# Kernel optimization log

Measured on AMD Instinct MI355X. Metric: run time of the kernel, lower is better.

Reference implementation:

```python
import jax, jax.numpy as jnp
import numpy as np
import math

B, N = 1, 768
C_S, C_Z, C_H, H, P_QK, P_V = 256, 128, 128, 8, 8, 12
EPS, INF, LN_EPS = 1e-8, 1e5, 1e-5


def _quat_to_rot(q):
    # q: [..., 4] normalized quaternion (w, x, y, z) -> [..., 3, 3]
    w, x, y, z = jnp.moveaxis(q, -1, 0)
    r = jnp.stack([
        1 - 2 * (y * y + z * z), 2 * (x * y - w * z), 2 * (x * z + w * y),
        2 * (x * y + w * z), 1 - 2 * (x * x + z * z), 2 * (y * z - w * x),
        2 * (x * z - w * y), 2 * (y * z + w * x), 1 - 2 * (x * x + y * y),
    ], axis=-1)
    return r.reshape(q.shape[:-1] + (3, 3))


def _ln(x, g, b):
    mu = x.mean(-1, keepdims=True)
    var = ((x - mu) ** 2).mean(-1, keepdims=True)
    return (x - mu) * jax.lax.rsqrt(var + LN_EPS) * g + b


def setup_inputs():
    key = jax.random.key(0)
    ks = jax.random.split(key, 20)
    inp = {}
    inp['s'] = jax.random.normal(ks[0], (B, N, C_S), jnp.float32)
    inp['p'] = jax.random.normal(ks[1], (B, N, N, C_Z), jnp.float32)
    q = jax.random.normal(ks[2], (B, N, 4), jnp.float32)
    inp['rot'] = _quat_to_rot(q / jnp.linalg.norm(q, axis=-1, keepdims=True))
    inp['trans'] = 10.0 * jax.random.normal(ks[3], (B, N, 3), jnp.float32)
    inp['mask'] = jnp.ones((B, N), jnp.float32)
    concat_dim = H * C_H + H * P_V * 4 + H * C_Z
    dims = {'q': (H * C_H, C_S), 'kv': (2 * H * C_H, C_S), 'qp': (H * P_QK * 3, C_S),
            'kvp': (H * (P_QK + P_V) * 3, C_S), 'pb': (H, C_Z), 'o': (C_S, concat_dim),
            't1': (C_S, C_S), 't2': (C_S, C_S), 't3': (C_S, C_S), 'bb': (6, C_S)}
    i = 4
    for nm, (do, di) in dims.items():
        k1, k2 = jax.random.split(ks[i]); i += 1
        inp['W' + nm] = 0.02 * jax.random.normal(k1, (do, di), jnp.float32)
        inp['b' + nm] = 0.02 * jax.random.normal(k2, (do,), jnp.float32)
    inp['head_w'] = 0.1 * jax.random.normal(ks[i], (H,), jnp.float32)
    inp['g1'] = jnp.ones((C_S,), jnp.float32)
    inp['be1'] = jnp.zeros((C_S,), jnp.float32)
    inp['g2'] = jnp.ones((C_S,), jnp.float32)
    inp['be2'] = jnp.zeros((C_S,), jnp.float32)
    return inp


def reference(s, p, rot, trans, mask, Wq, bq, Wkv, bkv, Wqp, bqp, Wkvp, bkvp,
              Wpb, bpb, Wo, bo, Wt1, bt1, Wt2, bt2, Wt3, bt3, Wbb, bbb,
              head_w, g1, be1, g2, be2):
    # ---------------- Invariant Point Attention ----------------
    q = (s @ Wq.T + bq).reshape(B, N, H, C_H)
    kv = (s @ Wkv.T + bkv).reshape(B, N, H, 2 * C_H)
    k, v = kv[..., :C_H], kv[..., C_H:]
    # points: linear output is coordinate-major (x-block, y-block, z-block)
    qp = (s @ Wqp.T + bqp).reshape(B, N, 3, H, P_QK)
    qp = jnp.einsum('bnij,bnjhp->bnhpi', rot, qp) + trans[:, :, None, None, :]
    kvp = (s @ Wkvp.T + bkvp).reshape(B, N, 3, H, P_QK + P_V)
    kvp = jnp.einsum('bnij,bnjhp->bnhpi', rot, kvp) + trans[:, :, None, None, :]
    kp, vp = kvp[..., :P_QK, :], kvp[..., P_QK:, :]
    bias_p = p @ Wpb.T + bpb  # [B,N,N,H]
    a = jnp.einsum('bihc,bjhc->bhij', q, k) * math.sqrt(1.0 / (3 * C_H))
    a = a + math.sqrt(1.0 / 3) * jnp.transpose(bias_p, (0, 3, 1, 2))
    d2 = ((qp[:, :, None] - kp[:, None]) ** 2).sum(-1)  # [B,N,N,H,Pqk]
    hw = jax.nn.softplus(head_w) * math.sqrt(1.0 / (3 * (P_QK * 9.0 / 2)))
    pt_att = -0.5 * (d2 * hw[None, None, None, :, None]).sum(-1)  # [B,N,N,H]
    m2 = mask[:, :, None] * mask[:, None, :]
    a = a + jnp.transpose(pt_att, (0, 3, 1, 2)) + (INF * (m2 - 1.0))[:, None]
    att = jax.nn.softmax(a, axis=-1)  # [B,H,N,N]
    o = jnp.einsum('bhij,bjhc->bihc', att, v).reshape(B, N, H * C_H)
    opt = jnp.einsum('bhij,bjhpx->bihpx', att, vp)  # [B,N,H,Pv,3] global
    opt = jnp.einsum('bnji,bnhpj->bnhpi', rot, opt - trans[:, :, None, None, :])
    opt_norm = jnp.sqrt((opt ** 2).sum(-1) + EPS).reshape(B, N, H * P_V)
    opt_flat = jnp.moveaxis(opt.reshape(B, N, H * P_V, 3), -1, -2).reshape(B, N, 3 * H * P_V)
    opair = jnp.einsum('bhij,bijz->bihz', att, p).reshape(B, N, H * C_Z)
    ipa_out = jnp.concatenate([o, opt_flat, opt_norm, opair], -1) @ Wo.T + bo
    # residual + dropout(eval: identity) + LayerNorm
    s1 = _ln(s + ipa_out, g1, be1)
    # ---------------- StructureTransition (1 layer) ----------------
    x = jax.nn.relu(s1 @ Wt1.T + bt1)
    x = jax.nn.relu(x @ Wt2.T + bt2)
    s2 = _ln(s1 + (x @ Wt3.T + bt3), g2, be2)
    # ---------------- BackboneUpdate + masked quaternion compose ----------------
    upd = (s2 @ Wbb.T + bbb) * mask[..., None]  # [B,N,6]
    qvec = jnp.concatenate([jnp.ones(upd.shape[:-1] + (1,), upd.dtype), upd[..., :3]], -1)
    qvec = qvec / jnp.linalg.norm(qvec, axis=-1, keepdims=True)
    rot_new = jnp.einsum('bnij,bnjk->bnik', rot, _quat_to_rot(qvec))
    trans_new = trans + jnp.einsum('bnij,bnj->bni', rot, upd[..., 3:])
    return (s2, rot_new, trans_new)
```

## Files before the change

### kernel.cpp

```cpp
#include <hip/hip_runtime.h>
#include <hip/hip_bf16.h>
#include <math.h>

#define NN 768
#define CS 256
#define CZ 128
#define CH 128
#define HH 8
#define PQK 8
#define PV 12
#define CONCAT 2432
#define ATT_HSTRIDE (768*768)

typedef __bf16 v8bf __attribute__((ext_vector_type(8)));
typedef __bf16 v4bf __attribute__((ext_vector_type(4)));
typedef float  v4f  __attribute__((ext_vector_type(4)));

__device__ inline unsigned short f2bf(float f) {
    union { float f; unsigned u; } v; v.f = f;
    unsigned r = v.u + 0x7FFFu + ((v.u >> 16) & 1u);
    return (unsigned short)(r >> 16);
}
__device__ inline float bf2f(unsigned short u) {
    union { unsigned u; float f; } v; v.u = ((unsigned)u) << 16; return v.f;
}

#define NCVT 9
struct CvtDesc {
    const float* src[NCVT];
    unsigned short* dst[NCVT];
    int nelem[NCVT];
    int blk_start[NCVT + 1];
};

__global__ __launch_bounds__(256) void cvt_many(CvtDesc d)
{
    int b = blockIdx.x;
    int seg = 0;
    #pragma unroll
    for (int i = 0; i < NCVT - 1; i++) if (b >= d.blk_start[i + 1]) seg = i + 1;
    int local = b - d.blk_start[seg];
    int base = local * 2048 + threadIdx.x;
    const float* s = d.src[seg];
    unsigned short* o = d.dst[seg];
    int n = d.nelem[seg];
    #pragma unroll
    for (int r = 0; r < 8; r++) {
        int idx = base + r * 256;
        if (idx < n) o[idx] = f2bf(s[idx]);
    }
}

struct ProjDesc {
    const unsigned short* W[4];
    const float* bias[4];
    unsigned short* dstb[4];
    float* dstf[4];
// ... 100 lines not shown
        v8bf b0 = *(const v8bf*)&Ws[wc + fr][fc];
        v8bf b1 = *(const v8bf*)&Ws[wc + 16 + fr][fc];
        acc[0][0] = __builtin_amdgcn_mfma_f32_16x16x32_bf16(a0, b0, acc[0][0], 0, 0, 0);
        acc[0][1] = __builtin_amdgcn_mfma_f32_16x16x32_bf16(a0, b1, acc[0][1], 0, 0, 0);
        acc[1][0] = __builtin_amdgcn_mfma_f32_16x16x32_bf16(a1, b0, acc[1][0], 0, 0, 0);
        acc[1][1] = __builtin_amdgcn_mfma_f32_16x16x32_bf16(a1, b1, acc[1][1], 0, 0, 0);
        __syncthreads();
    }
    int mrow = (lane >> 4) * 4;
    #pragma unroll
    for (int mi = 0; mi < 2; mi++) {
        #pragma unroll
        for (int ni = 0; ni < 2; ni++) {
            int d = bd + wc + ni * 16 + fr;
            if (d < D) {
                #pragma unroll
                for (int r = 0; r < 4; r++) {
                    int m = bi + wr + mi * 16 + mrow + r;
                    float v = acc[mi][ni][r];
                    if (SPLITK > 1) {
                        atomicAdd(&C[(size_t)m * ldc + d], v);
                    } else {
                        v += bias[d];
                        if (RELU) v = fmaxf(v, 0.f);
                        if (MODE != 2) C[(size_t)m * ldc + d] = v;
                        if (MODE >= 1) Cb[(size_t)m * ldc + d] = f2bf(v);
                    }
                }
            }
        }
    }
}

__global__ __launch_bounds__(256) void ipa_init_kernel(
    const float* __restrict__ bo, float* __restrict__ ipa)
{
    ipa[blockIdx.x * 256 + threadIdx.x] = bo[threadIdx.x];
}

__global__ void rotate_kernel(
    const float* __restrict__ qpraw, const float* __restrict__ kvpraw,
    const float* __restrict__ rot, const float* __restrict__ trans,
    unsigned short* __restrict__ qph, unsigned short* __restrict__ qpl,
    unsigned short* __restrict__ kph, unsigned short* __restrict__ kpl,
    unsigned short* __restrict__ Vc)
{
    int id = blockIdx.x*256 + threadIdx.x;
    if (id >= NN*HH*28) return;
    int i = id / (HH*28);
    int rem = id % (HH*28);
    int h = rem / 28;
    int idx = rem % 28;
    const float* R = rot + i*9;
    const float* T = trans + i*3;
    float s0, s1, s2;
    if (idx < 8) {
        s0 = qpraw[i*192 +   0 + h*8 + idx];
        s1 = qpraw[i*192 +  64 + h*8 + idx];
        s2 = qpraw[i*192 + 128 + h*8 + idx];
    } else {
        int pp = idx - 8;
        s0 = kvpraw[i*480 +   0 + h*20 + pp];
        s1 = kvpraw[i*480 + 160 + h*20 + pp];
        s2 = kvpraw[i*480 + 320 + h*20 + pp];
    }
    float ov[3];
    ov[0] = R[0]*s0 + R[1]*s1 + R[2]*s2 + T[0];
    ov[1] = R[3]*s0 + R[4]*s1 + R[5]*s2 + T[1];
    ov[2] = R[6]*s0 + R[7]*s1 + R[8]*s2 + T[2];
    if (idx < 8) {
        #pragma unroll
        for (int x = 0; x < 3; x++) {
            unsigned short hi = f2bf(ov[x]);
            qph[i*256 + h*32 + idx*3 + x] = hi;
            qpl[i*256 + h*32 + idx*3 + x] = f2bf(ov[x] - bf2f(hi));
        }
        if (idx == 0) {
            #pragma unroll
            for (int m = 24; m < 32; m++) { qph[i*256+h*32+m] = 0; qpl[i*256+h*32+m] = 0; }
        }
    } else if (idx < 16) {
        int pp = idx - 8;
        #pragma unroll
        for (int x = 0; x < 3; x++) {
            unsigned short hi = f2bf(ov[x]);
            kph[i*256 + h*32 + pp*3 + x] = hi;
            kpl[i*256 + h*32 + pp*3 + x] = f2bf(ov[x] - bf2f(hi));
        }
        if (idx == 8) {
            #pragma unroll
            for (int m = 24; m < 32; m++) { kph[i*256+h*32+m] = 0; kpl[i*256+h*32+m] = 0; }
        }
    } else {
        int ppv = idx - 16;
        #pragma unroll
        for (int x = 0; x < 3; x++)
            Vc[((size_t)h*192 + 128 + ppv*3 + x)*768 + i] = f2bf(ov[x]);
    }
}

__global__ __launch_bounds__(256) void vtrans_kernel(
    const unsigned short* __restrict__ kv_bf, unsigned short* __restrict__ Vc)
{
    __shared__ unsigned short tile[32][136];
    int h = blockIdx.x & 7, jt = blockIdx.x >> 3;
    int t = threadIdx.x;
    int r = t >> 3, c0 = (t & 7) * 16;
    const unsigned short* src = kv_bf + (size_t)(jt*32 + r)*2048 + h*256 + 128 + c0;
    *(int4*)&tile[r][c0]     = *(const int4*)src;
    *(int4*)&tile[r][c0 + 8] = *(const int4*)(src + 8);
    __syncthreads();
    int c = t >> 1, jh = (t & 1) * 16;
    unsigned short tmp[16];
    #pragma unroll
    for (int k = 0; k < 16; k++) tmp[k] = tile[jh + k][c];
    unsigned short* dst = Vc + ((size_t)h*192 + c)*768 + jt*32 + jh;
    *(int4*)dst       = *(int4*)&tmp[0];
    *(int4*)(dst + 8) = *(int4*)&tmp[8];
}

__global__ __launch_bounds__(256) void logits_mfma(
    const unsigned short* __restrict__ q_bf, const unsigned short* __restrict__ kv_bf,
    const unsigned short* __restrict__ qph, const unsigned short* __restrict__ qpl,
    const unsigned short* __restrict__ kph, const unsigned short* __restrict__ kpl,
    const float* __restrict__ mask, const float* __restrict__ head_w,
    float* __restrict__ att)
{
    __shared__ unsigned short Qs[64][136];
    __shared__ unsigned short Ks[64][136];
    __shared__ unsigned short Aph[64][40], Apl[64][40], Bph[64][40], Bpl[64][40];
    __shared__ float Qss[64], Kss[64], Mi[64], Mj[64];
    int h = blockIdx.z;
    int i0 = blockIdx.y * 64, j0 = blockIdx.x * 64;
    int tid = threadIdx.x, lane = tid & 63, wid = tid >> 6;
    int wr = (wid >> 1) * 32, wc = (wid & 1) * 32;
    int r = tid >> 2, cq = (tid & 3) * 32;
    const unsigned short* qg = q_bf  + (size_t)(i0 + r)*1024 + h*128 + cq;
    const unsigned short* kg = kv_bf + (size_t)(j0 + r)*2048 + h*256 + cq;
    #pragma unroll
    for (int kk = 0; kk < 4; kk++) {
        *(int4*)&Qs[r][cq + kk*8] = *(const int4*)(qg + kk*8);
        *(int4*)&Ks[r][cq + kk*8] = *(const int4*)(kg + kk*8);
    }
    int cp = (tid & 3) * 8;
    *(int4*)&Aph[r][cp] = *(const int4*)(qph + (size_t)(i0 + r)*256 + h*32 + cp);
    *(int4*)&Apl[r][cp] = *(const int4*)(qpl + (size_t)(i0 + r)*256 + h*32 + cp);
    *(int4*)&Bph[r][cp] = *(const int4*)(kph + (size_t)(j0 + r)*256 + h*32 + cp);
    *(int4*)&Bpl[r][cp] = *(const int4*)(kpl + (size_t)(j0 + r)*256 + h*32 + cp);
    if (tid < 64) {
        Mi[tid] = mask[i0 + tid];
        Mj[tid] = mask[j0 + tid];
    }
    __syncthreads();
    if (tid < 64) {
        float qs2 = 0.f, ks2 = 0.f;
        #pragma unroll
        for (int m = 0; m < 24; m++) {
            float qv = bf2f(Aph[tid][m]) + bf2f(Apl[tid][m]);
            float kv = bf2f(Bph[tid][m]) + bf2f(Bpl[tid][m]);
// ... 12 lines not shown
        aqk[0][0] = __builtin_amdgcn_mfma_f32_16x16x32_bf16(a0, b0, aqk[0][0], 0, 0, 0);
        aqk[0][1] = __builtin_amdgcn_mfma_f32_16x16x32_bf16(a0, b1, aqk[0][1], 0, 0, 0);
        aqk[1][0] = __builtin_amdgcn_mfma_f32_16x16x32_bf16(a1, b0, aqk[1][0], 0, 0, 0);
        aqk[1][1] = __builtin_amdgcn_mfma_f32_16x16x32_bf16(a1, b1, aqk[1][1], 0, 0, 0);
    }
    {
        v8bf ah0 = *(const v8bf*)&Aph[wr + fr][fc];
        v8bf ah1 = *(const v8bf*)&Aph[wr + 16 + fr][fc];
        v8bf al0 = *(const v8bf*)&Apl[wr + fr][fc];
        v8bf al1 = *(const v8bf*)&Apl[wr + 16 + fr][fc];
        v8bf bh0 = *(const v8bf*)&Bph[wc + fr][fc];
        v8bf bh1 = *(const v8bf*)&Bph[wc + 16 + fr][fc];
        v8bf bl0 = *(const v8bf*)&Bpl[wc + fr][fc];
        v8bf bl1 = *(const v8bf*)&Bpl[wc + 16 + fr][fc];
        ap[0][0] = __builtin_amdgcn_mfma_f32_16x16x32_bf16(ah0, bh0, ap[0][0], 0, 0, 0);
        ap[0][1] = __builtin_amdgcn_mfma_f32_16x16x32_bf16(ah0, bh1, ap[0][1], 0, 0, 0);
        ap[1][0] = __builtin_amdgcn_mfma_f32_16x16x32_bf16(ah1, bh0, ap[1][0], 0, 0, 0);
        ap[1][1] = __builtin_amdgcn_mfma_f32_16x16x32_bf16(ah1, bh1, ap[1][1], 0, 0, 0);
        ap[0][0] = __builtin_amdgcn_mfma_f32_16x16x32_bf16(ah0, bl0, ap[0][0], 0, 0, 0);
        ap[0][1] = __builtin_amdgcn_mfma_f32_16x16x32_bf16(ah0, bl1, ap[0][1], 0, 0, 0);
        ap[1][0] = __builtin_amdgcn_mfma_f32_16x16x32_bf16(ah1, bl0, ap[1][0], 0, 0, 0);
        ap[1][1] = __builtin_amdgcn_mfma_f32_16x16x32_bf16(ah1, bl1, ap[1][1], 0, 0, 0);
        ap[0][0] = __builtin_amdgcn_mfma_f32_16x16x32_bf16(al0, bh0, ap[0][0], 0, 0, 0);
        ap[0][1] = __builtin_amdgcn_mfma_f32_16x16x32_bf16(al0, bh1, ap[0][1], 0, 0, 0);
        ap[1][0] = __builtin_amdgcn_mfma_f32_16x16x32_bf16(al1, bh0, ap[1][0], 0, 0, 0);
        ap[1][1] = __builtin_amdgcn_mfma_f32_16x16x32_bf16(al1, bh1, ap[1][1], 0, 0, 0);
    }
    __syncthreads();
    float hx = head_w[h];
    float sp = (hx > 20.f) ? hx : log1pf(__expf(hx));
    float hw = sp * 0.09622504486493764f;
    const float scale_qk = 0.05103103630798288f;
    int mrow = (lane >> 4) * 4;
    #pragma unroll
    for (int mi = 0; mi < 2; mi++) {
        #pragma unroll
        for (int ni = 0; ni < 2; ni++) {
            int jl = wc + ni*16 + fr;
            #pragma unroll
            for (int rr = 0; rr < 4; rr++) {
                int il = wr + mi*16 + mrow + rr;
                size_t aidx = (size_t)h*ATT_HSTRIDE + (size_t)(i0 + il)*768 + (j0 + jl);
                att[aidx] = aqk[mi][ni][rr]*scale_qk + hw*ap[mi][ni][rr]
                          - 0.5f*hw*(Qss[il] + Kss[jl])
                          + 100000.0f*(Mi[il]*Mj[jl] - 1.0f);
            }
        }
    }
}

__global__ __launch_bounds__(256) void fused_p3_kernel(
    const float* __restrict__ att0,
    const float* __restrict__ p,
    const float* __restrict__ Wpb, const float* __restrict__ bpb,
    unsigned short* __restrict__ att_bf,
    float* __restrict__ linv,
    unsigned short* __restrict__ concat)
{
    __shared__ unsigned short ptile[64][132];
    __shared__ unsigned short wt[16][72];
    __shared__ float bpb_s[8], m8[8], inv_s[8], lsum_w[4][8];

    int i = blockIdx.x;
    int tid = threadIdx.x, lane = tid & 63, wid = tid >> 6;
    int fr = lane & 15, fc = (lane >> 4) * 8;
    int mrow = (lane >> 4) * 4;

    for (int idx = tid; idx < 16*72; idx += 256) ((unsigned short*)wt)[idx] = 0;
    if (tid < 8) bpb_s[tid] = bpb[tid];

    v8bf aW[4];
    #pragma unroll
    for (int ks = 0; ks < 4; ks++) {
        v8bf v = {};
        if (fr < 8) {
            const float* wp = Wpb + fr*128 + ks*32 + fc;
            float4 w0 = *(const float4*)wp;
            float4 w1 = *(const float4*)(wp + 4);
            v[0] = (__bf16)w0.x; v[1] = (__bf16)w0.y; v[2] = (__bf16)w0.z; v[3] = (__bf16)w0.w;
            v[4] = (__bf16)w1.x; v[5] = (__bf16)w1.y; v[6] = (__bf16)w1.z; v[7] = (__bf16)w1.w;
        }
        aW[ks] = v;
    }

    {
        const float* abase = att0 + (size_t)i*768;
        #pragma unroll
        for (int hh = 0; hh < 2; hh++) {
            int h = wid*2 + hh;
            const float* row = abase + (size_t)h*ATT_HSTRIDE;
            float m = -3.0e38f;
            #pragma unroll
            for (int e = 0; e < 12; e++) m = fmaxf(m, row[lane + e*64]);
            #pragma unroll
            for (int d2 = 1; d2 < 64; d2 <<= 1) m = fmaxf(m, __shfl_xor(m, d2));
            if (lane == 0) m8[h] = m;
        }
    }
    __syncthreads();
    float m0a[4], m0b[4];
    #pragma unroll
    for (int r = 0; r < 4; r++) { m0a[r] = m8[r]; m0b[r] = m8[4 + r]; }
    float m0l[4];
    #pragma unroll
    for (int r = 0; r < 4; r++) m0l[r] = (mrow == 0) ? m0a[r] : m0b[r];

    const float* pbase = p + (size_t)i*98304;
    float4 pfA[4], pfB[4];
    #pragma unroll
    for (int r = 0; r < 4; r++) {
        int idx = r*256 + tid;
        const float* src = pbase + (idx >> 4)*128 + (idx & 15)*8;
        pfA[r] = *(const float4*)src;
        pfB[r] = *(const float4*)(src + 4);
    }

    v4f accD[2] = {};
    float lacc[4] = {0.f, 0.f, 0.f, 0.f};
    const float sqrt13 = 0.57735026918962576f;
    bool expo = (mrow < 8);

    for (int t64 = 0; t64 < 12; t64++) {
        int j0 = t64 * 64;
        #pragma unroll
        for (int r = 0; r < 4; r++) {
            int idx = r*256 + tid;
            int j = idx >> 4, zo = (idx & 15) * 8;
            v4bf lo, hi;
            lo[0] = (__bf16)pfA[r].x; lo[1] = (__bf16)pfA[r].y;
            lo[2] = (__bf16)pfA[r].z; lo[3] = (__bf16)pfA[r].w;
            hi[0] = (__bf16)pfB[r].x; hi[1] = (__bf16)pfB[r].y;
            hi[2] = (__bf16)pfB[r].z; hi[3] = (__bf16)pfB[r].w;
            *(v4bf*)&ptile[j][zo]     = lo;
            *(v4bf*)&ptile[j][zo + 4] = hi;
        }
        if (t64 < 11) {
            int j0n = j0 + 64;
            #pragma unroll
            for (int r = 0; r < 4; r++) {
                int idx = r*256 + tid;
                const float* src = pbase + (size_t)(j0n + (idx >> 4))*128 + (idx & 15)*8;
                pfA[r] = *(const float4*)src;
                pfB[r] = *(const float4*)(src + 4);
            }
        }
        __syncthreads();

        float a0v[4];
        if (expo) {
            int j = 16*wid + fr;
            #pragma unroll
            for (int r = 0; r < 4; r++)
                a0v[r] = att0[((size_t)(mrow + r)*768 + i)*768 + j0 + j];
        }

        v4f bd = {};
        #pragma unroll
        for (int ks = 0; ks < 4; ks++) {
            int c = ks*32 + fc;
            v4bf blo = *(const v4bf*)&ptile[16*wid + fr][c];
            v4bf bhi = *(const v4bf*)&ptile[16*wid + fr][c + 4];
            v8bf b;
            b[0]=blo[0]; b[1]=blo[1]; b[2]=blo[2]; b[3]=blo[3];
            b[4]=bhi[0]; b[5]=bhi[1]; b[6]=bhi[2]; b[7]=bhi[3];
            bd = __builtin_amdgcn_mfma_f32_16x16x32_bf16(aW[ks], b, bd, 0, 0, 0);
        }

        if (expo) {
            int j = 16*wid + fr;
            float w8[4];
            #pragma unroll
            for (int r = 0; r < 4; r++) {
                int h = mrow + r;
                float L = a0v[r] + sqrt13*(bd[r] + bpb_s[h]);
// ... 8 lines not shown
            }
            #pragma unroll
            for (int m = 1; m < 16; m <<= 1) {
                #pragma unroll
                for (int r = 0; r < 4; r++) w8[r] += __shfl_xor(w8[r], m);
            }
            #pragma unroll
            for (int r = 0; r < 4; r++) lacc[r] += w8[r];
        }
        __syncthreads();

        #pragma unroll
        for (int mm = 0; mm < 2; mm++) {
            int zcol = (2*wid + mm)*16 + fr;
            #pragma unroll
            for (int ks = 0; ks < 2; ks++) {
                v8bf b;
                #pragma unroll
                for (int kk = 0; kk < 8; kk++)
                    b[kk] = *(const __bf16*)&ptile[ks*32 + fc + kk][zcol];
                v8bf a = *(const v8bf*)&wt[fr][ks*32 + fc];
                accD[mm] = __builtin_amdgcn_mfma_f32_16x16x32_bf16(a, b, accD[mm], 0, 0, 0);
            }
        }
        __syncthreads();
    }

    if (fr == 0 && expo) {
        #pragma unroll
        for (int r = 0; r < 4; r++) lsum_w[wid][mrow + r] = lacc[r];
    }
    __syncthreads();
    if (tid < 8) {
        float l = lsum_w[0][tid] + lsum_w[1][tid] + lsum_w[2][tid] + lsum_w[3][tid];
        float iv = 1.0f / l;
        inv_s[tid] = iv;
        linv[(size_t)tid*768 + i] = iv;
    }
    __syncthreads();
    if (expo) {
        #pragma unroll
        for (int mm = 0; mm < 2; mm++) {
            int z = (2*wid + mm)*16 + fr;
            #pragma unroll
            for (int r = 0; r < 4; r++) {
                int h = mrow + r;
                concat[(size_t)i*CONCAT + 1408 + h*128 + z] = f2bf(accD[mm][r] * inv_s[h]);
            }
        }
    }
}

__global__ __launch_bounds__(256) void attvc_mfma(
    const unsigned short* __restrict__ att_bf, const unsigned short* __restrict__ Vc,
    const float* __restrict__ linv, const float* __restrict__ rot,
    const float* __restrict__ trans, unsigned short* __restrict__ concat)
{
    __shared__ unsigned short As[64][72];
    __shared__ unsigned short Bs[64][72];
    int h = blockIdx.z;
    int i0 = blockIdx.y * 64, nd0 = blockIdx.x * 64;
    int tid = threadIdx.x, lane = tid & 63, wid = tid >> 6;
    int wr = (wid >> 1) * 32, wc = (wid & 1) * 32;
    int r = tid >> 2, c8 = (tid & 3) * 16;
    int fr = lane & 15, fc = (lane >> 4) * 8;
    v4f acc[2][2] = {};
    for (int k0 = 0; k0 < 768; k0 += 64) {
        const unsigned short* ag = att_bf + ((size_t)h*768 + i0 + r)*768 + k0 + c8;
        const unsigned short* bg = Vc + ((size_t)h*192 + nd0 + r)*768 + k0 + c8;
        *(int4*)&As[r][c8]     = *(const int4*)ag;
        *(int4*)&As[r][c8 + 8] = *(const int4*)(ag + 8);
        *(int4*)&Bs[r][c8]     = *(const int4*)bg;
        *(int4*)&Bs[r][c8 + 8] = *(const int4*)(bg + 8);
        __syncthreads();
        #pragma unroll
        for (int ks = 0; ks < 2; ks++) {
            v8bf a0 = *(const v8bf*)&As[wr + fr][ks*32 + fc];
            v8bf a1 = *(const v8bf*)&As[wr + 16 + fr][ks*32 + fc];
            v8bf b0 = *(const v8bf*)&Bs[wc + fr][ks*32 + fc];
            v8bf b1 = *(const v8bf*)&Bs[wc + 16 + fr][ks*32 + fc];
            acc[0][0] = __builtin_amdgcn_mfma_f32_16x16x32_bf16(a0, b0, acc[0][0], 0, 0, 0);
            acc[0][1] = __builtin_amdgcn_mfma_f32_16x16x32_bf16(a0, b1, acc[0][1], 0, 0, 0);
// ... 32 lines not shown
                int c = wc + ni*16 + fr;
                if (c < 36) {
                    #pragma unroll
                    for (int rr = 0; rr < 4; rr++) {
                        int rl = wr + mi*16 + mrow + rr;
                        opt_s[rl*36 + c] = acc[mi][ni][rr] * lv[mi][rr];
                    }
                }
            }
        }
        __syncthreads();
        for (int it = tid; it < 768; it += 256) {
            int rl = it / 12, pp = it % 12;
            int i = i0 + rl;
            const float* R = rot + i*9;
            const float* T = trans + i*3;
            float y0 = opt_s[rl*36 + pp*3 + 0] - T[0];
            float y1 = opt_s[rl*36 + pp*3 + 1] - T[1];
            float y2 = opt_s[rl*36 + pp*3 + 2] - T[2];
            float o0 = R[0]*y0 + R[3]*y1 + R[6]*y2;
            float o1 = R[1]*y0 + R[4]*y1 + R[7]*y2;
            float o2 = R[2]*y0 + R[5]*y1 + R[8]*y2;
            float nrm = sqrtf(o0*o0 + o1*o1 + o2*o2 + 1e-8f);
            int hp = h*12 + pp;
            unsigned short* cb = concat + (size_t)i*CONCAT;
            cb[1024 +   0 + hp] = f2bf(o0);
            cb[1024 +  96 + hp] = f2bf(o1);
            cb[1024 + 192 + hp] = f2bf(o2);
            cb[1312 + hp] = f2bf(nrm);
        }
    }
}

template<int BF>
__global__ __launch_bounds__(256) void add_ln_kernel(
    const float* __restrict__ A, const float* __restrict__ Bv,
    const float* __restrict__ g, const float* __restrict__ be,
    float* __restrict__ out, unsigned short* __restrict__ outb)
{
    int i = blockIdx.x, t = threadIdx.x;
    float x = A[i*256 + t] + Bv[i*256 + t];
    __shared__ float red[4];
    float v = x;
    #pragma unroll
    for (int m = 1; m < 64; m <<= 1) v += __shfl_xor(v, m);
    if ((t & 63) == 0) red[t >> 6] = v;
    __syncthreads();
    float mu = (red[0] + red[1] + red[2] + red[3]) * (1.0f/256.0f);
    __syncthreads();
    float d = x - mu;
    float v2 = d*d;
    #pragma unroll
    for (int m = 1; m < 64; m <<= 1) v2 += __shfl_xor(v2, m);
    if ((t & 63) == 0) red[t >> 6] = v2;
    __syncthreads();
    float var = (red[0] + red[1] + red[2] + red[3]) * (1.0f/256.0f);
    float o = d * (1.0f/sqrtf(var + 1e-5f)) * g[t] + be[t];
    out[i*256 + t] = o;
    if (BF) outb[i*256 + t] = f2bf(o);
}

__global__ __launch_bounds__(256) void upd_frame_kernel(
    const float* __restrict__ s2, const float* __restrict__ Wbb,
    const float* __restrict__ bbb, const float* __restrict__ mask,
    const float* __restrict__ rot, const float* __restrict__ trans,
    float* __restrict__ rot_out, float* __restrict__ trans_out)
{
    int i = blockIdx.x, t = threadIdx.x;
    __shared__ float row[256];
    __shared__ float upd_s[6];
    row[t] = s2[i*256 + t];
    __syncthreads();
    if (t < 6) {
        float acc = bbb[t];
        #pragma unroll 8
        for (int c = 0; c < 256; c++) acc += row[c]*Wbb[t*256 + c];
        upd_s[t] = acc * mask[i];
    }
    __syncthreads();
    if (t == 0) {
        float u0 = upd_s[0], u1 = upd_s[1], u2 = upd_s[2];
        float t0 = upd_s[3], t1 = upd_s[4], t2 = upd_s[5];
        float n = sqrtf(1.f + u0*u0 + u1*u1 + u2*u2);
        float w = 1.f/n, x = u0/n, y = u1/n, z = u2/n;
        float R[3][3];
        R[0][0] = 1.f - 2.f*(y*y + z*z); R[0][1] = 2.f*(x*y - w*z);       R[0][2] = 2.f*(x*z + w*y);
        R[1][0] = 2.f*(x*y + w*z);       R[1][1] = 1.f - 2.f*(x*x + z*z); R[1][2] = 2.f*(y*z - w*x);
        R[2][0] = 2.f*(x*z - w*y);       R[2][1] = 2.f*(y*z + w*x);       R[2][2] = 1.f - 2.f*(x*x + y*y);
        const float* Ri = rot + i*9;
        #pragma unroll
        for (int a = 0; a < 3; a++) {
            #pragma unroll
            for (int b = 0; b < 3; b++) {
                float acc = 0.f;
                #pragma unroll
                for (int j = 0; j < 3; j++) acc += Ri[a*3+j]*R[j][b];
                rot_out[i*9 + a*3 + b] = acc;
            }
            trans_out[i*3 + a] = trans[i*3 + a] + Ri[a*3+0]*t0 + Ri[a*3+1]*t1 + Ri[a*3+2]*t2;
        }
    }
}

extern "C" void kernel_launch(void* const* d_in, const int* in_sizes, int n_in,
                              void* d_out, int out_size, void* d_ws, size_t ws_size,
                              hipStream_t stream)
{
    const float* s      = (const float*)d_in[0];
    const float* p      = (const float*)d_in[1];
    const float* rot    = (const float*)d_in[2];
    const float* trans  = (const float*)d_in[3];
    const float* mask   = (const float*)d_in[4];
    const float* Wq     = (const float*)d_in[5];
    const float* bq     = (const float*)d_in[6];
    const float* Wkv    = (const float*)d_in[7];
// ... 3 lines not shown
    const float* Wkvp   = (const float*)d_in[11];
    const float* bkvp   = (const float*)d_in[12];
    const float* Wpb    = (const float*)d_in[13];
    const float* bpb    = (const float*)d_in[14];
    const float* Wo     = (const float*)d_in[15];
    const float* bo     = (const float*)d_in[16];
    const float* Wt1    = (const float*)d_in[17];
    const float* bt1    = (const float*)d_in[18];
    const float* Wt2    = (const float*)d_in[19];
    const float* bt2    = (const float*)d_in[20];
    const float* Wt3    = (const float*)d_in[21];
    const float* bt3    = (const float*)d_in[22];
    const float* Wbb    = (const float*)d_in[23];
    const float* bbb    = (const float*)d_in[24];
    const float* head_w = (const float*)d_in[25];
    const float* g1     = (const float*)d_in[26];
    const float* be1    = (const float*)d_in[27];
    const float* g2     = (const float*)d_in[28];
    const float* be2    = (const float*)d_in[29];

    float* out = (float*)d_out;
    char*  wsb = (char*)d_ws;

    size_t off = 0;
    auto alloc = [&](size_t bytes) -> char* {
        char* ptr = wsb + off;
        off += (bytes + 255) & ~(size_t)255;
        return ptr;
    };
    float* qpraw   = (float*)alloc((size_t)NN*192*4);
    float* kvpraw  = (float*)alloc((size_t)NN*480*4);
    float* att     = (float*)alloc((size_t)8*768*768*4);
    float* ipa     = (float*)alloc((size_t)NN*256*4);
    float* s1      = (float*)alloc((size_t)NN*256*4);
    float* y3      = (float*)alloc((size_t)NN*256*4);
    float* linv    = (float*)alloc((size_t)8*768*4);
    unsigned short* s_bf    = (unsigned short*)alloc((size_t)NN*256*2);
    unsigned short* Wq_bf   = (unsigned short*)alloc((size_t)1024*256*2);
    unsigned short* Wkv_bf  = (unsigned short*)alloc((size_t)2048*256*2);
    unsigned short* Wqp_bf  = (unsigned short*)alloc((size_t)192*256*2);
    unsigned short* Wkvp_bf = (unsigned short*)alloc((size_t)480*256*2);
    unsigned short* Wo_bf   = (unsigned short*)alloc((size_t)256*2432*2);
    unsigned short* Wt1_bf  = (unsigned short*)alloc((size_t)256*256*2);
    unsigned short* Wt2_bf  = (unsigned short*)alloc((size_t)256*256*2);
    unsigned short* Wt3_bf  = (unsigned short*)alloc((size_t)256*256*2);
    unsigned short* q_bf    = (unsigned short*)alloc((size_t)NN*1024*2);
    unsigned short* kv_bf   = (unsigned short*)alloc((size_t)NN*2048*2);
    unsigned short* qph     = (unsigned short*)alloc((size_t)NN*256*2);
    unsigned short* qpl     = (unsigned short*)alloc((size_t)NN*256*2);
    unsigned short* kph     = (unsigned short*)alloc((size_t)NN*256*2);
    unsigned short* kpl     = (unsigned short*)alloc((size_t)NN*256*2);
    unsigned short* Vc      = (unsigned short*)alloc((size_t)8*192*768*2);
    unsigned short* att_bf  = (unsigned short*)alloc((size_t)8*768*768*2);
    unsigned short* concat  = (unsigned short*)alloc((size_t)NN*CONCAT*2);
    unsigned short* s1b     = (unsigned short*)alloc((size_t)NN*256*2);
    unsigned short* x1b     = (unsigned short*)alloc((size_t)NN*256*2);
    unsigned short* x2b     = (unsigned short*)alloc((size_t)NN*256*2);

    ipa_init_kernel<<<768, 256, 0, stream>>>(bo, ipa);

    CvtDesc cd;
    const float* csrc[NCVT]    = {s, Wq, Wkv, Wqp, Wkvp, Wo, Wt1, Wt2, Wt3};
    unsigned short* cdst[NCVT] = {s_bf, Wq_bf, Wkv_bf, Wqp_bf, Wkvp_bf, Wo_bf, Wt1_bf, Wt2_bf, Wt3_bf};
    int csz[NCVT] = {NN*256, 1024*256, 2048*256, 192*256, 480*256, 256*2432, 256*256, 256*256, 256*256};
    int cum = 0;
    for (int i2 = 0; i2 < NCVT; i2++) {
        cd.src[i2] = csrc[i2]; cd.dst[i2] = cdst[i2]; cd.nelem[i2] = csz[i2];
        cd.blk_start[i2] = cum;
        cum += (csz[i2] + 2047) / 2048;
    }
    cd.blk_start[NCVT] = cum;
    cvt_many<<<cum, 256, 0, stream>>>(cd);

    ProjDesc pd;
    pd.W[0] = Wq_bf;   pd.bias[0] = bq;   pd.dstb[0] = q_bf;   pd.dstf[0] = nullptr; pd.D[0] = 1024; pd.ldc[0] = 1024; pd.mode[0] = 2;
    pd.W[1] = Wkv_bf;  pd.bias[1] = bkv;  pd.dstb[1] = kv_bf;  pd.dstf[1] = nullptr; pd.D[1] = 2048; pd.ldc[1] = 2048; pd.mode[1] = 2;
    pd.W[2] = Wqp_bf;  pd.bias[2] = bqp;  pd.dstb[2] = nullptr; pd.dstf[2] = qpraw;  pd.D[2] = 192;  pd.ldc[2] = 192;  pd.mode[2] = 0;
    pd.W[3] = Wkvp_bf; pd.bias[3] = bkvp; pd.dstb[3] = nullptr; pd.dstf[3] = kvpraw; pd.D[3] = 480;  pd.ldc[3] = 480;  pd.mode[3] = 0;
    pd.blk_start[0] = 0; pd.blk_start[1] = 16; pd.blk_start[2] = 48; pd.blk_start[3] = 51; pd.blk_start[4] = 59;
    proj_all<<<dim3(59, 12), 256, 0, stream>>>(s_bf, pd);

    rotate_kernel<<<(NN*HH*28 + 255)/256, 256, 0, stream>>>(
        qpraw, kvpraw, rot, trans, qph, qpl, kph, kpl, Vc);
    vtrans_kernel<<<8*24, 256, 0, stream>>>(kv_bf, Vc);

    logits_mfma<<<dim3(12, 12, 8), 256, 0, stream>>>(
        q_bf, kv_bf, qph, qpl, kph, kpl, mask, head_w, att);
    fused_p3_kernel<<<768, 256, 0, stream>>>(att, p, Wpb, bpb, att_bf, linv, concat);

    attvc_mfma<<<dim3(3, 12, 8), 256, 0, stream>>>(att_bf, Vc, linv, rot, trans, concat);

    mfma_gemm<4,0,0><<<dim3(4,12,4), 256, 0, stream>>>(concat, Wo_bf, nullptr, ipa, nullptr, 256, 2432, 256);
    add_ln_kernel<1><<<768, 256, 0, stream>>>(s, ipa, g1, be1, s1, s1b);

    mfma_gemm<1,2,1><<<dim3(4,12), 256, 0, stream>>>(s1b, Wt1_bf, bt1, nullptr, x1b, 256, 256, 256);
    mfma_gemm<1,2,1><<<dim3(4,12), 256, 0, stream>>>(x1b, Wt2_bf, bt2, nullptr, x2b, 256, 256, 256);
    mfma_gemm<1,0,0><<<dim3(4,12), 256, 0, stream>>>(x2b, Wt3_bf, bt3, y3, nullptr, 256, 256, 256);
    add_ln_kernel<0><<<768, 256, 0, stream>>>(s1, y3, g2, be2, out, nullptr);

    upd_frame_kernel<<<768, 256, 0, stream>>>(out, Wbb, bbb, mask, rot, trans,
                                              out + (size_t)NN*256, out + (size_t)NN*256 + (size_t)NN*9);
}
```

Before: 195.1 us.

## Fuse prep and tail kernels, move row-max into logits, split pair pass

Merges the rotate and V-transpose kernels into one launch. The softmax row max is now computed inside the logits kernel through atomicMax on order-preserving encoded floats, so the pair kernel no longer rereads att for the max. The pair-bias/opair kernel is split over two j-halves for more parallelism, and a new reduce kernel combines the partial sums and outputs. The LN, transition MLP, LN and frame-update stages are fused into one 24-block tail kernel, and bias init is replaced by a memset with bo added in the tail. The changes cut launches and att traffic, but the tail runs on only 24 blocks and the split adds partial-sum buffers.

```diff
diff --git a/kernel.cpp b/kernel.cpp
--- a/kernel.cpp
+++ b/kernel.cpp
@@ -23,6 +23,14 @@
 }
 __device__ inline float bf2f(unsigned short u) {
     union { unsigned u; float f; } v; v.u = ((unsigned)u) << 16; return v.f;
+}
+__device__ inline unsigned encf(float f) {
+    unsigned u = __float_as_uint(f);
+    return (u >> 31) ? ~u : (u | 0x80000000u);
+}
+__device__ inline float decf(unsigned e) {
+    unsigned u = (e >> 31) ? (e & 0x7FFFFFFFu) : ~e;
+    return __uint_as_float(u);
 }
 
 #define NCVT 9
@@ -189,91 +197,85 @@
     }
 }
 
-__global__ __launch_bounds__(256) void ipa_init_kernel(
-    const float* __restrict__ bo, float* __restrict__ ipa)
-{
-    ipa[blockIdx.x * 256 + threadIdx.x] = bo[threadIdx.x];
-}
-
-__global__ void rotate_kernel(
+__global__ __launch_bounds__(256) void prep2_kernel(
     const float* __restrict__ qpraw, const float* __restrict__ kvpraw,
     const float* __restrict__ rot, const float* __restrict__ trans,
+    const unsigned short* __restrict__ kv_bf,
     unsigned short* __restrict__ qph, unsigned short* __restrict__ qpl,
     unsigned short* __restrict__ kph, unsigned short* __restrict__ kpl,
     unsigned short* __restrict__ Vc)
 {
-    int id = blockIdx.x*256 + threadIdx.x;
-    if (id >= NN*HH*28) return;
-    int i = id / (HH*28);
-    int rem = id % (HH*28);
-    int h = rem / 28;
-    int idx = rem % 28;
-    const float* R = rot + i*9;
-    const float* T = trans + i*3;
-    float s0, s1, s2;
-    if (idx < 8) {
-        s0 = qpraw[i*192 +   0 + h*8 + idx];
-        s1 = qpraw[i*192 +  64 + h*8 + idx];
-        s2 = qpraw[i*192 + 128 + h*8 + idx];
+    __shared__ unsigned short tile[32][136];
+    int bx = blockIdx.x;
+    int t = threadIdx.x;
+    if (bx < 672) {
+        int id = bx*256 + t;
+        int i = id / (HH*28);
+        int rem = id % (HH*28);
+        int h = rem / 28;
+        int idx = rem % 28;
+        const float* R = rot + i*9;
+        const float* T = trans + i*3;
+        float s0, s1, s2;
+        if (idx < 8) {
+            s0 = qpraw[i*192 +   0 + h*8 + idx];
+            s1 = qpraw[i*192 +  64 + h*8 + idx];
+            s2 = qpraw[i*192 + 128 + h*8 + idx];
+        } else {
+            int pp = idx - 8;
+            s0 = kvpraw[i*480 +   0 + h*20 + pp];
+            s1 = kvpraw[i*480 + 160 + h*20 + pp];
+            s2 = kvpraw[i*480 + 320 + h*20 + pp];
+        }
+        float ov[3];
+        ov[0] = R[0]*s0 + R[1]*s1 + R[2]*s2 + T[0];
+        ov[1] = R[3]*s0 + R[4]*s1 + R[5]*s2 + T[1];
+        ov[2] = R[6]*s0 + R[7]*s1 + R[8]*s2 + T[2];
+        if (idx < 8) {
+            #pragma unroll
+            for (int x = 0; x < 3; x++) {
+                unsigned short hi = f2bf(ov[x]);
+                qph[i*256 + h*32 + idx*3 + x] = hi;
+                qpl[i*256 + h*32 + idx*3 + x] = f2bf(ov[x] - bf2f(hi));
+            }
+            if (idx == 0) {
+                #pragma unroll
+                for (int m = 24; m < 32; m++) { qph[i*256+h*32+m] = 0; qpl[i*256+h*32+m] = 0; }
+            }
+        } else if (idx < 16) {
+            int pp = idx - 8;
+            #pragma unroll
+            for (int x = 0; x < 3; x++) {
+                unsigned short hi = f2bf(ov[x]);
+                kph[i*256 + h*32 + pp*3 + x] = hi;
+                kpl[i*256 + h*32 + pp*3 + x] = f2bf(ov[x] - bf2f(hi));
+            }
+            if (idx == 8) {
+                #pragma unroll
+                for (int m = 24; m < 32; m++) { kph[i*256+h*32+m] = 0; kpl[i*256+h*32+m] = 0; }
+            }
+        } else {
+            int ppv = idx - 16;
+            #pragma unroll
+            for (int x = 0; x < 3; x++)
+                Vc[((size_t)h*192 + 128 + ppv*3 + x)*768 + i] = f2bf(ov[x]);
+        }
     } else {
-        int pp = idx - 8;
-        s0 = kvpraw[i*480 +   0 + h*20 + pp];
-        s1 = kvpraw[i*480 + 160 + h*20 + pp];
-        s2 = kvpraw[i*480 + 320 + h*20 + pp];
-    }
-    float ov[3];
-    ov[0] = R[0]*s0 + R[1]*s1 + R[2]*s2 + T[0];
-    ov[1] = R[3]*s0 + R[4]*s1 + R[5]*s2 + T[1];
-    ov[2] = R[6]*s0 + R[7]*s1 + R[8]*s2 + T[2];
-    if (idx < 8) {
-        #pragma unroll
-        for (int x = 0; x < 3; x++) {
-            unsigned short hi = f2bf(ov[x]);
-            qph[i*256 + h*32 + idx*3 + x] = hi;
-            qpl[i*256 + h*32 + idx*3 + x] = f2bf(ov[x] - bf2f(hi));
-        }
-        if (idx == 0) {
-            #pragma unroll
-            for (int m = 24; m < 32; m++) { qph[i*256+h*32+m] = 0; qpl[i*256+h*32+m] = 0; }
-        }
-    } else if (idx < 16) {
-        int pp = idx - 8;
-        #pragma unroll
-        for (int x = 0; x < 3; x++) {
-            unsigned short hi = f2bf(ov[x]);
-            kph[i*256 + h*32 + pp*3 + x] = hi;
-            kpl[i*256 + h*32 + pp*3 + x] = f2bf(ov[x] - bf2f(hi));
-        }
-        if (idx == 8) {
-            #pragma unroll
-            for (int m = 24; m < 32; m++) { kph[i*256+h*32+m] = 0; kpl[i*256+h*32+m] = 0; }
-        }
-    } else {
-        int ppv = idx - 16;
-        #pragma unroll
-        for (int x = 0; x < 3; x++)
-            Vc[((size_t)h*192 + 128 + ppv*3 + x)*768 + i] = f2bf(ov[x]);
-    }
-}
-
-__global__ __launch_bounds__(256) void vtrans_kernel(
-    const unsigned short* __restrict__ kv_bf, unsigned short* __restrict__ Vc)
-{
-    __shared__ unsigned short tile[32][136];
-    int h = blockIdx.x & 7, jt = blockIdx.x >> 3;
-    int t = threadIdx.x;
-    int r = t >> 3, c0 = (t & 7) * 16;
-    const unsigned short* src = kv_bf + (size_t)(jt*32 + r)*2048 + h*256 + 128 + c0;
-    *(int4*)&tile[r][c0]     = *(const int4*)src;
-    *(int4*)&tile[r][c0 + 8] = *(const int4*)(src + 8);
-    __syncthreads();
-    int c = t >> 1, jh = (t & 1) * 16;
-    unsigned short tmp[16];
-    #pragma unroll
-    for (int k = 0; k < 16; k++) tmp[k] = tile[jh + k][c];
-    unsigned short* dst = Vc + ((size_t)h*192 + c)*768 + jt*32 + jh;
-    *(int4*)dst       = *(int4*)&tmp[0];
-    *(int4*)(dst + 8) = *(int4*)&tmp[8];
+        int bx2 = bx - 672;
+        int h = bx2 & 7, jt = bx2 >> 3;
+        int r = t >> 3, c0 = (t & 7) * 16;
+        const unsigned short* src = kv_bf + (size_t)(jt*32 + r)*2048 + h*256 + 128 + c0;
+        *(int4*)&tile[r][c0]     = *(const int4*)src;
+        *(int4*)&tile[r][c0 + 8] = *(const int4*)(src + 8);
+        __syncthreads();
+        int c = t >> 1, jh = (t & 1) * 16;
+        unsigned short tmp[16];
+        #pragma unroll
+        for (int k = 0; k < 16; k++) tmp[k] = tile[jh + k][c];
+        unsigned short* dst = Vc + ((size_t)h*192 + c)*768 + jt*32 + jh;
+        *(int4*)dst       = *(int4*)&tmp[0];
+        *(int4*)(dst + 8) = *(int4*)&tmp[8];
+    }
 }
 
 __global__ __launch_bounds__(256) void logits_mfma(
@@ -281,7 +283,7 @@
     const unsigned short* __restrict__ qph, const unsigned short* __restrict__ qpl,
     const unsigned short* __restrict__ kph, const unsigned short* __restrict__ kpl,
     const float* __restrict__ mask, const float* __restrict__ head_w,
-    float* __restrict__ att)
+    float* __restrict__ att, unsigned* __restrict__ m0enc)
 {
     __shared__ unsigned short Qs[64][136];
     __shared__ unsigned short Ks[64][136];
@@ -360,6 +362,7 @@
     float hw = sp * 0.09622504486493764f;
     const float scale_qk = 0.05103103630798288f;
     int mrow = (lane >> 4) * 4;
+    float val[2][2][4];
     #pragma unroll
     for (int mi = 0; mi < 2; mi++) {
         #pragma unroll
@@ -368,34 +371,54 @@
             #pragma unroll
             for (int rr = 0; rr < 4; rr++) {
                 int il = wr + mi*16 + mrow + rr;
-                size_t aidx = (size_t)h*ATT_HSTRIDE + (size_t)(i0 + il)*768 + (j0 + jl);
-                att[aidx] = aqk[mi][ni][rr]*scale_qk + hw*ap[mi][ni][rr]
-                          - 0.5f*hw*(Qss[il] + Kss[jl])
-                          + 100000.0f*(Mi[il]*Mj[jl] - 1.0f);
-            }
-        }
-    }
-}
-
-__global__ __launch_bounds__(256) void fused_p3_kernel(
+                float v = aqk[mi][ni][rr]*scale_qk + hw*ap[mi][ni][rr]
+                        - 0.5f*hw*(Qss[il] + Kss[jl])
+                        + 100000.0f*(Mi[il]*Mj[jl] - 1.0f);
+                val[mi][ni][rr] = v;
+                att[(size_t)h*ATT_HSTRIDE + (size_t)(i0 + il)*768 + (j0 + jl)] = v;
+            }
+        }
+    }
+    #pragma unroll
+    for (int mi = 0; mi < 2; mi++) {
+        #pragma unroll
+        for (int rr = 0; rr < 4; rr++) {
+            float m = fmaxf(val[mi][0][rr], val[mi][1][rr]);
+            #pragma unroll
+            for (int d2 = 1; d2 < 16; d2 <<= 1) m = fmaxf(m, __shfl_xor(m, d2));
+            if (fr == 0) {
+                int il = wr + mi*16 + mrow + rr;
+                atomicMax(&m0enc[h*768 + i0 + il], encf(m));
+            }
+        }
+    }
+}
+
+__global__ __launch_bounds__(256) void fused_p3s_kernel(
     const float* __restrict__ att0,
     const float* __restrict__ p,
     const float* __restrict__ Wpb, const float* __restrict__ bpb,
+    const unsigned* __restrict__ m0enc,
     unsigned short* __restrict__ att_bf,
-    float* __restrict__ linv,
-    unsigned short* __restrict__ concat)
+    float* __restrict__ lpart,
+    float* __restrict__ opart)
 {
     __shared__ unsigned short ptile[64][132];
     __shared__ unsigned short wt[16][72];
-    __shared__ float bpb_s[8], m8[8], inv_s[8], lsum_w[4][8];
+    __shared__ float bpb_s[8], m8[8], lsum_w[4][8];
 
     int i = blockIdx.x;
+    int half = blockIdx.y;
+    int jbase = half * 384;
     int tid = threadIdx.x, lane = tid & 63, wid = tid >> 6;
     int fr = lane & 15, fc = (lane >> 4) * 8;
     int mrow = (lane >> 4) * 4;
 
     for (int idx = tid; idx < 16*72; idx += 256) ((unsigned short*)wt)[idx] = 0;
-    if (tid < 8) bpb_s[tid] = bpb[tid];
+    if (tid < 8) {
+        bpb_s[tid] = bpb[tid];
+        m8[tid] = decf(m0enc[tid*768 + i]);
+    }
 
     v8bf aW[4];
     #pragma unroll
@@ -410,30 +433,12 @@
         }
         aW[ks] = v;
     }
-
-    {
-        const float* abase = att0 + (size_t)i*768;
-        #pragma unroll
-        for (int hh = 0; hh < 2; hh++) {
-            int h = wid*2 + hh;
-            const float* row = abase + (size_t)h*ATT_HSTRIDE;
-            float m = -3.0e38f;
-            #pragma unroll
-            for (int e = 0; e < 12; e++) m = fmaxf(m, row[lane + e*64]);
-            #pragma unroll
-            for (int d2 = 1; d2 < 64; d2 <<= 1) m = fmaxf(m, __shfl_xor(m, d2));
-            if (lane == 0) m8[h] = m;
-        }
-    }
     __syncthreads();
-    float m0a[4], m0b[4];
-    #pragma unroll
-    for (int r = 0; r < 4; r++) { m0a[r] = m8[r]; m0b[r] = m8[4 + r]; }
     float m0l[4];
     #pragma unroll
-    for (int r = 0; r < 4; r++) m0l[r] = (mrow == 0) ? m0a[r] : m0b[r];
-
-    const float* pbase = p + (size_t)i*98304;
+    for (int r = 0; r < 4; r++) m0l[r] = (mrow == 0) ? m8[r] : m8[4 + r];
+
+    const float* pbase = p + (size_t)i*98304 + (size_t)jbase*128;
     float4 pfA[4], pfB[4];
     #pragma unroll
     for (int r = 0; r < 4; r++) {
@@ -448,8 +453,8 @@
     const float sqrt13 = 0.57735026918962576f;
     bool expo = (mrow < 8);
 
-    for (int t64 = 0; t64 < 12; t64++) {
-        int j0 = t64 * 64;
+    for (int t64 = 0; t64 < 6; t64++) {
+        int j0 = jbase + t64 * 64;
         #pragma unroll
         for (int r = 0; r < 4; r++) {
             int idx = r*256 + tid;
@@ -462,12 +467,11 @@
             *(v4bf*)&ptile[j][zo]     = lo;
             *(v4bf*)&ptile[j][zo + 4] = hi;
         }
-        if (t64 < 11) {
-            int j0n = j0 + 64;
+        if (t64 < 5) {
             #pragma unroll
             for (int r = 0; r < 4; r++) {
                 int idx = r*256 + tid;
-                const float* src = pbase + (size_t)(j0n + (idx >> 4))*128 + (idx & 15)*8;
+                const float* src = pbase + (size_t)((t64+1)*64 + (idx >> 4))*128 + (idx & 15)*8;
                 pfA[r] = *(const float4*)src;
                 pfB[r] = *(const float4*)(src + 4);
             }
@@ -542,22 +546,41 @@
     }
     __syncthreads();
     if (tid < 8) {
-        float l = lsum_w[0][tid] + lsum_w[1][tid] + lsum_w[2][tid] + lsum_w[3][tid];
-        float iv = 1.0f / l;
-        inv_s[tid] = iv;
-        linv[(size_t)tid*768 + i] = iv;
-    }
-    __syncthreads();
+        lpart[(size_t)(half*8 + tid)*768 + i] =
+            lsum_w[0][tid] + lsum_w[1][tid] + lsum_w[2][tid] + lsum_w[3][tid];
+    }
     if (expo) {
+        float* ob = opart + (size_t)(half*768 + i)*1024;
         #pragma unroll
         for (int mm = 0; mm < 2; mm++) {
             int z = (2*wid + mm)*16 + fr;
             #pragma unroll
-            for (int r = 0; r < 4; r++) {
-                int h = mrow + r;
-                concat[(size_t)i*CONCAT + 1408 + h*128 + z] = f2bf(accD[mm][r] * inv_s[h]);
-            }
-        }
+            for (int r = 0; r < 4; r++)
+                ob[(mrow + r)*128 + z] = accD[mm][r];
+        }
+    }
+}
+
+__global__ __launch_bounds__(256) void preduce_kernel(
+    const float* __restrict__ lpart, const float* __restrict__ opart,
+    float* __restrict__ linv, unsigned short* __restrict__ concat)
+{
+    __shared__ float inv_s[8];
+    int i = blockIdx.x, t = threadIdx.x;
+    if (t < 8) {
+        float l = lpart[(size_t)t*768 + i] + lpart[(size_t)(8 + t)*768 + i];
+        float iv = 1.0f / l;
+        inv_s[t] = iv;
+        linv[(size_t)t*768 + i] = iv;
+    }
+    __syncthreads();
+    const float* o0 = opart + (size_t)i*1024;
+    const float* o1 = opart + (size_t)(768 + i)*1024;
+    #pragma unroll
+    for (int k = 0; k < 4; k++) {
+        int c = t + k*256;
+        float s = o0[c] + o1[c];
+        concat[(size_t)i*CONCAT + 1408 + c] = f2bf(s * inv_s[c >> 7]);
     }
 }
 
@@ -656,55 +679,147 @@
     }
 }
 
-template<int BF>
-__global__ __launch_bounds__(256) void add_ln_kernel(
-    const float* __restrict__ A, const float* __restrict__ Bv,
-    const float* __restrict__ g, const float* __restrict__ be,
-    float* __restrict__ out, unsigned short* __restrict__ outb)
+__global__ __launch_bounds__(256) void tail_kernel(
+    const float* __restrict__ s, const float* __restrict__ ipa,
+    const float* __restrict__ bo,
+    const float* __restrict__ g1, const float* __restrict__ be1,
+    const unsigned short* __restrict__ Wt1, const float* __restrict__ bt1,
+    const unsigned short* __restrict__ Wt2, const float* __restrict__ bt2,
+    const unsigned short* __restrict__ Wt3, const float* __restrict__ bt3,
+    const float* __restrict__ g2, const float* __restrict__ be2,
+    const float* __restrict__ Wbb, const float* __restrict__ bbb,
+    const float* __restrict__ mask,
+    const float* __restrict__ rot, const float* __restrict__ trans,
+    float* __restrict__ out, float* __restrict__ rot_out, float* __restrict__ trans_out)
 {
-    int i = blockIdx.x, t = threadIdx.x;
-    float x = A[i*256 + t] + Bv[i*256 + t];
-    __shared__ float red[4];
-    float v = x;
-    #pragma unroll
-    for (int m = 1; m < 64; m <<= 1) v += __shfl_xor(v, m);
-    if ((t & 63) == 0) red[t >> 6] = v;
+    __shared__ float s1f[32][257];
+    __shared__ unsigned short Ab[32][264];
+    __shared__ float upd_s[32][6];
+    int i0 = blockIdx.x * 32;
+    int tid = threadIdx.x, lane = tid & 63, wid = tid >> 6;
+    int fr = lane & 15, fc = (lane >> 4) * 8, mrow = (lane >> 4) * 4;
+
+    int r = tid >> 3, cg = (tid & 7) * 32;
+    {
+        float xv[32];
+        float sum = 0.f, sq = 0.f;
+        #pragma unroll
+        for (int q = 0; q < 8; q++) {
+            float4 a = *(const float4*)&s[(size_t)(i0 + r)*256 + cg + q*4];
+            float4 b = *(const float4*)&ipa[(size_t)(i0 + r)*256 + cg + q*4];
+            float4 c = *(const float4*)&bo[cg + q*4];
+            float v0 = a.x + b.x + c.x, v1 = a.y + b.y + c.y;
+            float v2 = a.z + b.z + c.z, v3 = a.w + b.w + c.w;
+            xv[q*4+0] = v0; xv[q*4+1] = v1; xv[q*4+2] = v2; xv[q*4+3] = v3;
+            sum += v0 + v1 + v2 + v3;
+            sq  += v0*v0 + v1*v1 + v2*v2 + v3*v3;
+        }
+        #pragma unroll
+        for (int d = 1; d < 8; d <<= 1) { sum += __shfl_xor(sum, d); sq += __shfl_xor(sq, d); }
+        float mu = sum * (1.0f/256.0f);
+        float var = sq * (1.0f/256.0f) - mu*mu;
+        float rsig = 1.0f / sqrtf(var + 1e-5f);
+        #pragma unroll
+        for (int c = 0; c < 32; c++) {
+            float o = (xv[c] - mu) * rsig * g1[cg + c] + be1[cg + c];
+            s1f[r][cg + c] = o;
+            Ab[r][cg + c] = f2bf(o);
+        }
+    }
     __syncthreads();
-    float mu = (red[0] + red[1] + red[2] + red[3]) * (1.0f/256.0f);
+
+    const unsigned short* Ws[3] = {Wt1, Wt2, Wt3};
+    const float* Bs[3] = {bt1, bt2, bt3};
+    #pragma unroll
+    for (int stage = 0; stage < 3; stage++) {
+        const unsigned short* W = Ws[stage];
+        const float* bias = Bs[stage];
+        v4f acc[2][4] = {};
+        #pragma unroll
+        for (int k0 = 0; k0 < 8; k0++) {
+            v8bf a0 = *(const v8bf*)&Ab[fr][k0*32 + fc];
+            v8bf a1 = *(const v8bf*)&Ab[16 + fr][k0*32 + fc];
+            #pragma unroll
+            for (int n = 0; n < 4; n++) {
+                int d = wid*64 + n*16 + fr;
+                v8bf b = *(const v8bf*)&W[(size_t)d*256 + k0*32 + fc];
+                acc[0][n] = __builtin_amdgcn_mfma_f32_16x16x32_bf16(a0, b, acc[0][n], 0, 0, 0);
+                acc[1][n] = __builtin_amdgcn_mfma_f32_16x16x32_bf16(a1, b, acc[1][n], 0, 0, 0);
+            }
+        }
+        __syncthreads();
+        if (stage < 2) {
+            #pragma unroll
+            for (int mi = 0; mi < 2; mi++) {
+                #pragma unroll
+                for (int n = 0; n < 4; n++) {
+                    int d = wid*64 + n*16 + fr;
+                    #pragma unroll
+                    for (int rr = 0; rr < 4; rr++) {
+                        int m = mi*16 + mrow + rr;
+                        Ab[m][d] = f2bf(fmaxf(acc[mi][n][rr] + bias[d], 0.f));
+                    }
+                }
+            }
+        } else {
+            #pragma unroll
+            for (int mi = 0; mi < 2; mi++) {
+                #pragma unroll
+                for (int n = 0; n < 4; n++) {
+                    int d = wid*64 + n*16 + fr;
+                    #pragma unroll
+                    for (int rr = 0; rr < 4; rr++) {
+                        int m = mi*16 + mrow + rr;
+                        s1f[m][d] += acc[mi][n][rr] + bias[d];
+                    }
+                }
+            }
+        }
+        __syncthreads();
+    }
+
+    {
+        float xv[32];
+        float sum = 0.f, sq = 0.f;
+        #pragma unroll
+        for (int c = 0; c < 32; c++) {
+            float v = s1f[r][cg + c];
+            xv[c] = v; sum += v; sq += v*v;
+        }
+        #pragma unroll
+        for (int d = 1; d < 8; d <<= 1) { sum += __shfl_xor(sum, d); sq += __shfl_xor(sq, d); }
+        float mu = sum * (1.0f/256.0f);
+        float var = sq * (1.0f/256.0f) - mu*mu;
+        float rsig = 1.0f / sqrtf(var + 1e-5f);
+        float o4[32];
+        #pragma unroll
+        for (int c = 0; c < 32; c++)
+            o4[c] = (xv[c] - mu) * rsig * g2[cg + c] + be2[cg + c];
+        #pragma unroll
+        for (int q = 0; q < 8; q++) {
+            float4 w; w.x = o4[q*4]; w.y = o4[q*4+1]; w.z = o4[q*4+2]; w.w = o4[q*4+3];
+            *(float4*)&out[(size_t)(i0 + r)*256 + cg + q*4] = w;
+        }
+        __syncthreads();
+        #pragma unroll
+        for (int c = 0; c < 32; c++) s1f[r][cg + c] = o4[c];
+    }
     __syncthreads();
-    float d = x - mu;
-    float v2 = d*d;
-    #pragma unroll
-    for (int m = 1; m < 64; m <<= 1) v2 += __shfl_xor(v2, m);
-    if ((t & 63) == 0) red[t >> 6] = v2;
+
+    if (tid < 192) {
+        int rr = tid / 6, d = tid % 6;
+        float acc = bbb[d];
+        const float* wb = Wbb + d*256;
+        #pragma unroll 8
+        for (int c = 0; c < 256; c++) acc += s1f[rr][c] * wb[c];
+        upd_s[rr][d] = acc * mask[i0 + rr];
+    }
     __syncthreads();
-    float var = (red[0] + red[1] + red[2] + red[3]) * (1.0f/256.0f);
-    float o = d * (1.0f/sqrtf(var + 1e-5f)) * g[t] + be[t];
-    out[i*256 + t] = o;
-    if (BF) outb[i*256 + t] = f2bf(o);
-}
-
-__global__ __launch_bounds__(256) void upd_frame_kernel(
-    const float* __restrict__ s2, const float* __restrict__ Wbb,
-    const float* __restrict__ bbb, const float* __restrict__ mask,
-    const float* __restrict__ rot, const float* __restrict__ trans,
-    float* __restrict__ rot_out, float* __restrict__ trans_out)
-{
-    int i = blockIdx.x, t = threadIdx.x;
-    __shared__ float row[256];
-    __shared__ float upd_s[6];
-    row[t] = s2[i*256 + t];
-    __syncthreads();
-    if (t < 6) {
-        float acc = bbb[t];
-        #pragma unroll 8
-        for (int c = 0; c < 256; c++) acc += row[c]*Wbb[t*256 + c];
-        upd_s[t] = acc * mask[i];
-    }
-    __syncthreads();
-    if (t == 0) {
-        float u0 = upd_s[0], u1 = upd_s[1], u2 = upd_s[2];
-        float t0 = upd_s[3], t1 = upd_s[4], t2 = upd_s[5];
+
+    if (tid < 32) {
+        int i = i0 + tid;
+        float u0 = upd_s[tid][0], u1 = upd_s[tid][1], u2 = upd_s[tid][2];
+        float t0 = upd_s[tid][3], t1 = upd_s[tid][4], t2 = upd_s[tid][5];
         float n = sqrtf(1.f + u0*u0 + u1*u1 + u2*u2);
         float w = 1.f/n, x = u0/n, y = u1/n, z = u2/n;
         float R[3][3];
@@ -774,9 +889,10 @@
     float* kvpraw  = (float*)alloc((size_t)NN*480*4);
     float* att     = (float*)alloc((size_t)8*768*768*4);
     float* ipa     = (float*)alloc((size_t)NN*256*4);
-    float* s1      = (float*)alloc((size_t)NN*256*4);
-    float* y3      = (float*)alloc((size_t)NN*256*4);
     float* linv    = (float*)alloc((size_t)8*768*4);
+    float* lpart   = (float*)alloc((size_t)16*768*4);
+    float* opart   = (float*)alloc((size_t)2*768*1024*4);
+    unsigned* m0enc = (unsigned*)alloc((size_t)8*768*4);
     unsigned short* s_bf    = (unsigned short*)alloc((size_t)NN*256*2);
     unsigned short* Wq_bf   = (unsigned short*)alloc((size_t)1024*256*2);
     unsigned short* Wkv_bf  = (unsigned short*)alloc((size_t)2048*256*2);
@@ -795,11 +911,9 @@
     unsigned short* Vc      = (unsigned short*)alloc((size_t)8*192*768*2);
     unsigned short* att_bf  = (unsigned short*)alloc((size_t)8*768*768*2);
     unsigned short* concat  = (unsigned short*)alloc((size_t)NN*CONCAT*2);
-    unsigned short* s1b     = (unsigned short*)alloc((size_t)NN*256*2);
-    unsigned short* x1b     = (unsigned short*)alloc((size_t)NN*256*2);
-    unsigned short* x2b     = (unsigned short*)alloc((size_t)NN*256*2);
-
-    ipa_init_kernel<<<768, 256, 0, stream>>>(bo, ipa);
+
+    hipMemsetAsync(ipa, 0, (size_t)NN*256*4, stream);
+    hipMemsetAsync(m0enc, 0, (size_t)8*768*4, stream);
 
     CvtDesc cd;
     const float* csrc[NCVT]    = {s, Wq, Wkv, Wqp, Wkvp, Wo, Wt1, Wt2, Wt3};
@@ -822,24 +936,22 @@
     pd.blk_start[0] = 0; pd.blk_start[1] = 16; pd.blk_start[2] = 48; pd.blk_start[3] = 51; pd.blk_start[4] = 59;
     proj_all<<<dim3(59, 12), 256, 0, stream>>>(s_bf, pd);
 
-    rotate_kernel<<<(NN*HH*28 + 255)/256, 256, 0, stream>>>(
-        qpraw, kvpraw, rot, trans, qph, qpl, kph, kpl, Vc);
-    vtrans_kernel<<<8*24, 256, 0, stream>>>(kv_bf, Vc);
+    prep2_kernel<<<672 + 192, 256, 0, stream>>>(
+        qpraw, kvpraw, rot, trans, kv_bf, qph, qpl, kph, kpl, Vc);
 
     logits_mfma<<<dim3(12, 12, 8), 256, 0, stream>>>(
-        q_bf, kv_bf, qph, qpl, kph, kpl, mask, head_w, att);
-    fused_p3_kernel<<<768, 256, 0, stream>>>(att, p, Wpb, bpb, att_bf, linv, concat);
+        q_bf, kv_bf, qph, qpl, kph, kpl, mask, head_w, att, m0enc);
+
+    fused_p3s_kernel<<<dim3(768, 2), 256, 0, stream>>>(
+        att, p, Wpb, bpb, m0enc, att_bf, lpart, opart);
+    preduce_kernel<<<768, 256, 0, stream>>>(lpart, opart, linv, concat);
 
     attvc_mfma<<<dim3(3, 12, 8), 256, 0, stream>>>(att_bf, Vc, linv, rot, trans, concat);
 
     mfma_gemm<4,0,0><<<dim3(4,12,4), 256, 0, stream>>>(concat, Wo_bf, nullptr, ipa, nullptr, 256, 2432, 256);
-    add_ln_kernel<1><<<768, 256, 0, stream>>>(s, ipa, g1, be1, s1, s1b);
-
-    mfma_gemm<1,2,1><<<dim3(4,12), 256, 0, stream>>>(s1b, Wt1_bf, bt1, nullptr, x1b, 256, 256, 256);
-    mfma_gemm<1,2,1><<<dim3(4,12), 256, 0, stream>>>(x1b, Wt2_bf, bt2, nullptr, x2b, 256, 256, 256);
-    mfma_gemm<1,0,0><<<dim3(4,12), 256, 0, stream>>>(x2b, Wt3_bf, bt3, y3, nullptr, 256, 256, 256);
-    add_ln_kernel<0><<<768, 256, 0, stream>>>(s1, y3, g2, be2, out, nullptr);
-
-    upd_frame_kernel<<<768, 256, 0, stream>>>(out, Wbb, bbb, mask, rot, trans,
-                                              out + (size_t)NN*256, out + (size_t)NN*256 + (size_t)NN*9);
-}
+
+    tail_kernel<<<24, 256, 0, stream>>>(
+        s, ipa, bo, g1, be1, Wt1_bf, bt1, Wt2_bf, bt2, Wt3_bf, bt3,
+        g2, be2, Wbb, bbb, mask, rot, trans,
+        out, out + (size_t)NN*256, out + (size_t)NN*256 + (size_t)NN*9);
+}
```

Result: no change. 192.7 us (-1.2%).
